# Performance work log

Hardware: AMD Instinct MI355X
Metric: run time of the kernel (lower is better)

Reference implementation:

```python
import jax, jax.numpy as jnp
import numpy as np

INPUT_DIM = 1024
HIDDEN_DIM = 2048
NUM_EMB = 4096
EMB_DIM = 256
N = 65536


def setup_inputs() -> dict:
    key = jax.random.key(0)
    ks = jax.random.split(key, 10)
    s = lambda fan_in: 1.0 / np.sqrt(fan_in)
    return {
        "x": jax.random.normal(ks[0], (N, INPUT_DIM), dtype=jnp.float32),
        # encoder: Linear(input_dim, hidden) -> ReLU -> Linear(hidden, emb)
        "W1": jax.random.uniform(ks[1], (INPUT_DIM, HIDDEN_DIM), jnp.float32, -s(INPUT_DIM), s(INPUT_DIM)),
        "b1": jax.random.uniform(ks[2], (HIDDEN_DIM,), jnp.float32, -s(INPUT_DIM), s(INPUT_DIM)),
        "W2": jax.random.uniform(ks[3], (HIDDEN_DIM, EMB_DIM), jnp.float32, -s(HIDDEN_DIM), s(HIDDEN_DIM)),
        "b2": jax.random.uniform(ks[4], (EMB_DIM,), jnp.float32, -s(HIDDEN_DIM), s(HIDDEN_DIM)),
        # codebook (nn.Embedding weight)
        "codebook": jax.random.normal(ks[5], (NUM_EMB, EMB_DIM), dtype=jnp.float32),
        # decoder: Linear(emb, hidden) -> ReLU -> Linear(hidden, input_dim)
        "W3": jax.random.uniform(ks[6], (EMB_DIM, HIDDEN_DIM), jnp.float32, -s(EMB_DIM), s(EMB_DIM)),
        "b3": jax.random.uniform(ks[7], (HIDDEN_DIM,), jnp.float32, -s(EMB_DIM), s(EMB_DIM)),
        "W4": jax.random.uniform(ks[8], (HIDDEN_DIM, INPUT_DIM), jnp.float32, -s(HIDDEN_DIM), s(HIDDEN_DIM)),
        "b4": jax.random.uniform(ks[9], (INPUT_DIM,), jnp.float32, -s(HIDDEN_DIM), s(HIDDEN_DIM)),
    }


def reference(x, W1, b1, W2, b2, codebook, W3, b3, W4, b4):
    # encoder
    h = jax.nn.relu(x @ W1 + b1)
    encoded = h @ W2 + b2                      # [N, E]
    # cdist (squared form; argmin is identical to Euclidean argmin)
    enc_sq = jnp.sum(encoded * encoded, axis=-1, keepdims=True)   # [N, 1]
    cb_sq = jnp.sum(codebook * codebook, axis=-1)                 # [K]
    d2 = enc_sq - 2.0 * (encoded @ codebook.T) + cb_sq            # [N, K]
    indices = jnp.argmin(d2, axis=-1)                             # [N]
    quantized = codebook[indices]                                 # [N, E]
    # decoder
    h2 = jax.nn.relu(quantized @ W3 + b3)
    decoded = h2 @ W4 + b4
    return (quantized, decoded)
```

## Files before the change

### kernel.cpp

```cpp
#include <hip/hip_runtime.h>

#define N_ROWS 65536
#define IN_DIM 1024
#define HID    2048
#define EMB    256
#define NCODE  4096

typedef __attribute__((ext_vector_type(8))) short bf16x8;
typedef __attribute__((ext_vector_type(4))) float f32x4;

__device__ __forceinline__ unsigned short f2bf(float v) {
    unsigned u = __float_as_uint(v);
    u += 0x7FFFu + ((u >> 16) & 1u);
    return (unsigned short)(u >> 16);
}
__device__ __forceinline__ float bf2f(unsigned short h) {
    return __uint_as_float(((unsigned)h) << 16);
}
__device__ __forceinline__ void gload16(const unsigned short* g, unsigned short* l) {
    __builtin_amdgcn_global_load_lds(
        (const __attribute__((address_space(1))) unsigned int*)g,
        (__attribute__((address_space(3))) unsigned int*)l, 16, 0, 0);
}

template<int SPLIT>
__global__ __launch_bounds__(256) void k_conv_w(
    const float* __restrict__ src, unsigned short* __restrict__ dh,
    unsigned short* __restrict__ dl, int NC, int nkt)
{
    const int t = threadIdx.x;
    const int nt = blockIdx.x, kt = blockIdx.y;
    const int kk = t >> 2, j4 = (t & 3) << 2;
    const int k0 = kt << 6, n0 = nt << 4;
    float4 v = *(const float4*)(src + (size_t)(k0 + kk) * NC + n0 + j4);
    size_t tb = ((size_t)nt * nkt + kt) * 1024 + ((kk >> 3) * 128) + (kk & 7);
    float vv[4] = {v.x, v.y, v.z, v.w};
    #pragma unroll
    for (int j = 0; j < 4; ++j) {
        unsigned short h = f2bf(vv[j]);
        dh[tb + (size_t)(j4 + j) * 8] = h;
        if (SPLIT) dl[tb + (size_t)(j4 + j) * 8] = f2bf(vv[j] - bf2f(h));
    }
}

__global__ __launch_bounds__(256) void k_conv_cb(
    const float* __restrict__ cb, unsigned short* __restrict__ ch,
    unsigned short* __restrict__ cl_, float* __restrict__ halfsq)
{
    const int t = threadIdx.x;
    const int ct = blockIdx.x;
    const int cl = t >> 4, f = t & 15;
    const int code = (ct << 4) + cl;
    float ssq = 0.f;
    #pragma unroll
    for (int it = 0; it < 4; ++it) {
        const int k4 = (f << 2) + (it << 6);
        float4 v = *(const float4*)(cb + (size_t)code * EMB + k4);
        ssq += v.x * v.x + v.y * v.y + v.z * v.z + v.w * v.w;
        size_t tb = ((size_t)(ct * 4 + (k4 >> 6))) * 1024 + ((k4 >> 3) & 7) * 128 + cl * 8 + (k4 & 7);
        ushort4 h = { f2bf(v.x), f2bf(v.y), f2bf(v.z), f2bf(v.w) };
        *(ushort4*)&ch[tb] = h;
        ushort4 lo = { f2bf(v.x - bf2f(h.x)), f2bf(v.y - bf2f(h.y)),
                       f2bf(v.z - bf2f(h.z)), f2bf(v.w - bf2f(h.w)) };
        *(ushort4*)&cl_[tb] = lo;
    }
    #pragma unroll
    for (int off = 1; off <= 8; off <<= 1) ssq += __shfl_xor(ssq, off);
    if (f == 0) halfsq[code] = 0.5f * ssq;
}

template<int SPLIT, int AFMT, int OUTT>
__global__ __launch_bounds__(512, 2) void k_layer2(
    const float* __restrict__ A, const unsigned short* __restrict__ At, int a_nkt,
    int lda, int K,
    const unsigned short* __restrict__ Bh, const unsigned short* __restrict__ Bl,
    int b_nkt, const float* __restrict__ bias, int biasoff,
    float* __restrict__ out, unsigned short* __restrict__ outt,
    int outw, int relu, int init, int ny_log2)
{
    constexpr int AL = 8192;
    constexpr int BH = SPLIT ? 16384 : 8192;
    __shared__ __align__(16) unsigned short s_mem[32768];

    const int t = threadIdx.x;
    const int id = blockIdx.x;
    const int m_low = id & 7, rest = id >> 3;
    const int nb = rest & ((1 << ny_log2) - 1);
    const int m0 = (((rest >> ny_log2) << 3) | m_low) * 128;
    const int nb0 = nb * 256;
    const int lane = t & 63, wv = t >> 6;
    const int wm = wv >> 2, wn = wv & 3;
    const int g = lane >> 4, rr = lane & 15;

    f32x4 acc[4][4];
    #pragma unroll
    for (int mi = 0; mi < 4; ++mi)
        #pragma unroll
        for (int ni = 0; ni < 4; ++ni) acc[mi][ni] = (f32x4){0.f, 0.f, 0.f, 0.f};

    for (int kc = 0; kc < K; kc += 64) {
        const int ktile = kc >> 6;
        #pragma unroll
        for (int jj = 0; jj < 2; ++jj) {
            const int j = wv * 2 + jj;
            const size_t gt = ((size_t)(nb0 / 16 + j) * b_nkt + ktile) * 1024;
            #pragma unroll
            for (int half = 0; half < 2; ++half)
                gload16(Bh + gt + half * 512 + lane * 8,
                        &s_mem[BH + j * 1024 + half * 512]);
        }
        if (AFMT == 0) {
            #pragma unroll
            for (int it = 0; it < 4; ++it) {
                int f = t + (it << 9);
                int r = f >> 4, k4 = (f & 15) << 2;
                float4 v = *(const float4*)(A + (size_t)(m0 + r) * lda + kc + k4);
                int mt = r >> 4, rl = r & 15, kb = k4 >> 3, e = k4 & 7;
                int addr = mt * 1024 + kb * 128 + ((rl ^ kb) << 3) + e;
                ushort4 hi, lo;
                hi.x = f2bf(v.x); hi.y = f2bf(v.y); hi.z = f2bf(v.z); hi.w = f2bf(v.w);
                *(ushort4*)&s_mem[addr] = hi;
                if (SPLIT) {
                    lo.x = f2bf(v.x - bf2f(hi.x)); lo.y = f2bf(v.y - bf2f(hi.y));
                    lo.z = f2bf(v.z - bf2f(hi.z)); lo.w = f2bf(v.w - bf2f(hi.w));
                    *(ushort4*)&s_mem[AL + addr] = lo;
                }
            }
        } else {
            const size_t gt = ((size_t)(m0 / 16 + wv) * a_nkt + ktile) * 1024;
            #pragma unroll
            for (int half = 0; half < 2; ++half)
                gload16(At + gt + half * 512 + lane * 8,
                        &s_mem[wv * 1024 + half * 512]);
        }
        __syncthreads();
        __builtin_amdgcn_s_setprio(1);
        #pragma unroll
        for (int s = 0; s < 2; ++s) {
            const int kb = (s << 2) + g;
            bf16x8 a_h[4], a_l[4], b_h[4], b_l[4];
            #pragma unroll
            for (int i = 0; i < 4; ++i) {
                int arow = (AFMT == 0) ? (((rr ^ kb) & 15) << 3) : (rr << 3);
                int aaddr = (wm * 4 + i) * 1024 + kb * 128 + arow;
                a_h[i] = *(const bf16x8*)&s_mem[aaddr];
                if (SPLIT) a_l[i] = *(const bf16x8*)&s_mem[AL + aaddr];
                int baddr = (wn * 4 + i) * 1024 + kb * 128 + (rr << 3);
                b_h[i] = *(const bf16x8*)&s_mem[BH + baddr];
                if (SPLIT)
                    b_l[i] = *(const bf16x8*)(Bl +
                        ((size_t)(nb0 / 16 + wn * 4 + i) * b_nkt + ktile) * 1024
                        + kb * 128 + (rr << 3));
            }
            #pragma unroll
            for (int mi = 0; mi < 4; ++mi)
                #pragma unroll
                for (int ni = 0; ni < 4; ++ni) {
                    acc[mi][ni] = __builtin_amdgcn_mfma_f32_16x16x32_bf16(a_h[mi], b_h[ni], acc[mi][ni], 0, 0, 0);
                    if (SPLIT) {
                        acc[mi][ni] = __builtin_amdgcn_mfma_f32_16x16x32_bf16(a_l[mi], b_h[ni], acc[mi][ni], 0, 0, 0);
                        acc[mi][ni] = __builtin_amdgcn_mfma_f32_16x16x32_bf16(a_h[mi], b_l[ni], acc[mi][ni], 0, 0, 0);
                    }
                }
        }
        __builtin_amdgcn_s_setprio(0);
        __syncthreads();
    }

    if (OUTT == 0) {
        float* sf = (float*)s_mem;
        for (int rm = 0; rm < 2; ++rm) {
            if (wm == rm) {
                #pragma unroll
                for (int mi = 0; mi < 4; ++mi)
                    #pragma unroll
                    for (int ni = 0; ni < 4; ++ni)
                        #pragma unroll
                        for (int rg = 0; rg < 4; ++rg)
                            sf[(mi * 16 + g * 4 + rg) * 256 + wn * 64 + ni * 16 + rr] = acc[mi][ni][rg];
            }
            __syncthreads();
            #pragma unroll
            for (int it = 0; it < 8; ++it) {
                int f = t + (it << 9);
                int r = f >> 6, c4 = (f & 63) << 2;
                float4 v = *(const float4*)&sf[r * 256 + c4];
                int gr = m0 + rm * 64 + r, gc = nb0 + c4;
                float* op = out + (size_t)gr * outw + gc;
                if (init) {
                    v.x += bias[biasoff + gc + 0]; v.y += bias[biasoff + gc + 1];
                    v.z += bias[biasoff + gc + 2]; v.w += bias[biasoff + gc + 3];
                } else {
                    float4 o = *(const float4*)op;
                    v.x += o.x; v.y += o.y; v.z += o.z; v.w += o.w;
                }
                if (relu) {
                    v.x = fmaxf(v.x, 0.f); v.y = fmaxf(v.y, 0.f);
                    v.z = fmaxf(v.z, 0.f); v.w = fmaxf(v.w, 0.f);
                }
                *(float4*)op = v;
            }
            __syncthreads();
        }
    } else {
        #pragma unroll
        for (int mi = 0; mi < 4; ++mi)
            #pragma unroll
            for (int ni = 0; ni < 4; ++ni) {
                const int c = wn * 64 + ni * 16 + rr;
                float bb = bias[biasoff + nb0 + c];
                #pragma unroll
                for (int rg = 0; rg < 4; ++rg) {
                    float v = acc[mi][ni][rg] + bb;
                    if (relu) v = fmaxf(v, 0.f);
                    int addr = ((wm * 4 + mi) * 4 + wn) * 1024
                             + (ni * 2 + (rr >> 3)) * 128 + (g * 4 + rg) * 8 + (rr & 7);
                    s_mem[addr] = f2bf(v);
                }
            }
        __syncthreads();
        #pragma unroll
        for (int it = 0; it < 8; ++it) {
            int f = t + (it << 9);
            int tl = f >> 7, w8 = f & 127;
            size_t gaddr = ((size_t)(m0 / 16 + (tl >> 2)) * outw + nb0 / 64 + (tl & 3)) * 1024;
            *(float4*)(outt + gaddr + w8 * 8) = *(const float4*)&s_mem[tl * 1024 + w8 * 8];
        }
    }
}

__global__ __launch_bounds__(512, 4) void k_dist(
    float* encq, const unsigned short* __restrict__ ch,
    const unsigned short* __restrict__ cl,
    const float* __restrict__ hsq, const float* __restrict__ cb)
{
    __shared__ __align__(16) unsigned short s_cb[2][16384];
    __shared__ int s_c1[128], s_c2[128];

    const int t = threadIdx.x;
    const int lane = t & 63, wv = t >> 6;
    const int g = lane >> 4, rr = lane & 15;
    const int r0 = blockIdx.x * 128;

    bf16x8 eh[8], el[8];
    {
        const float* ep = encq + (size_t)(r0 + wv * 16 + rr) * EMB + g * 8;
        #pragma unroll
        for (int s = 0; s < 8; ++s) {
            float4 v0 = *(const float4*)(ep + s * 32);
            float4 v1 = *(const float4*)(ep + s * 32 + 4);
            float vv[8] = {v0.x, v0.y, v0.z, v0.w, v1.x, v1.y, v1.z, v1.w};
            bf16x8 a, b;
            #pragma unroll
            for (int j = 0; j < 8; ++j) {
                unsigned short h = f2bf(vv[j]);
                a[j] = (short)h;
                b[j] = (short)f2bf(vv[j] - bf2f(h));
            }
            eh[s] = a; el[s] = b;
        }
    }
    float b1v[4], b2v[4]; int i1v[4], i2v[4];
    #pragma unroll
    for (int r2 = 0; r2 < 4; ++r2) { b1v[r2] = -1e30f; b2v[r2] = -1e30f; i1v[r2] = 0; i2v[r2] = 0; }

    #define STAGE(buf, c)                                                              \
        {                                                                              \
            const unsigned short* gh_ = ch + (size_t)(c) * 8192 + wv * 1024;           \
            const unsigned short* gl_ = cl + (size_t)(c) * 8192 + wv * 1024;           \
            _Pragma("unroll")                                                          \
            for (int i_ = 0; i_ < 2; ++i_) {                                           \
                gload16(gh_ + i_ * 512 + lane * 8, &s_cb[buf][wv * 1024 + i_ * 512]);  \
                gload16(gl_ + i_ * 512 + lane * 8, &s_cb[buf][8192 + wv * 1024 + i_ * 512]); \
            }                                                                          \
        }

    #define COMPUTE(cur, c, hv_)                                                       \
        {                                                                              \
            f32x4 ahh[2], ahl[2], alh[2];                                              \
            _Pragma("unroll")                                                          \
            for (int ci = 0; ci < 2; ++ci) {                                           \
                ahh[ci] = (f32x4){0.f, 0.f, 0.f, 0.f};                                 \
                ahl[ci] = (f32x4){0.f, 0.f, 0.f, 0.f};                                 \
                alh[ci] = (f32x4){0.f, 0.f, 0.f, 0.f};                                 \
            }                                                                          \
            __builtin_amdgcn_s_setprio(1);                                             \
            _Pragma("unroll")                                                          \
            for (int s = 0; s < 8; ++s) {                                              \
                const int ktile = s >> 1, kb = ((s & 1) << 2) + g;                     \
                _Pragma("unroll")                                                      \
                for (int ci = 0; ci < 2; ++ci) {                                       \
                    const int off = (ci * 4 + ktile) * 1024 + kb * 128 + rr * 8;       \
                    bf16x8 bh = *(const bf16x8*)&s_cb[cur][off];                       \
                    bf16x8 bl = *(const bf16x8*)&s_cb[cur][8192 + off];                \
                    ahh[ci] = __builtin_amdgcn_mfma_f32_16x16x32_bf16(eh[s], bh, ahh[ci], 0, 0, 0); \
                    ahl[ci] = __builtin_amdgcn_mfma_f32_16x16x32_bf16(eh[s], bl, ahl[ci], 0, 0, 0); \
                    alh[ci] = __builtin_amdgcn_mfma_f32_16x16x32_bf16(el[s], bh, alh[ci], 0, 0, 0); \
                }                                                                      \
            }                                                                          \
            __builtin_amdgcn_s_setprio(0);                                             \
            _Pragma("unroll")                                                          \
            for (int ci = 0; ci < 2; ++ci) {                                           \
                f32x4 av = ahh[ci] + ahl[ci] + alh[ci];                                \
                const int code = ((c) << 5) + (ci << 4) + rr;                          \
                const float hs = __shfl(hv_, ci * 16 + rr);                            \
                _Pragma("unroll")                                                      \
                for (int r2 = 0; r2 < 4; ++r2) {                                       \
                    float v = av[r2] - hs;                                             \
                    bool bt1 = (v > b1v[r2]) || (v == b1v[r2] && code < i1v[r2]);      \
                    bool bt2 = (v > b2v[r2]) || (v == b2v[r2] && code < i2v[r2]);      \
                    if (bt1) { b2v[r2] = b1v[r2]; i2v[r2] = i1v[r2]; b1v[r2] = v; i1v[r2] = code; } \
                    else if (bt2) { b2v[r2] = v; i2v[r2] = code; }                     \
                }                                                                      \
            }                                                                          \
        }

    STAGE(0, 0)
    int cur = 0;
    for (int c = 0; c < 127; ++c) {
        STAGE(cur ^ 1, c + 1)
        float hv_ = hsq[(c << 5) + (lane & 31)];
        asm volatile("s_waitcnt vmcnt(5)" ::: "memory");
        __builtin_amdgcn_s_barrier();
        __builtin_amdgcn_sched_barrier(0);
        COMPUTE(cur, c, hv_)
        asm volatile("" ::: "memory");
        __builtin_amdgcn_s_barrier();
        cur ^= 1;
    }
    {
        float hv_ = hsq[(127 << 5) + (lane & 31)];
        asm volatile("s_waitcnt vmcnt(0)" ::: "memory");
        __builtin_amdgcn_s_barrier();
        __builtin_amdgcn_sched_barrier(0);
        COMPUTE(cur, 127, hv_)
    }
    #undef STAGE
    #undef COMPUTE

    #pragma unroll
    for (int off = 1; off <= 8; off <<= 1) {
        #pragma unroll
        for (int r2 = 0; r2 < 4; ++r2) {
            float ob1 = __shfl_xor(b1v[r2], off), ob2 = __shfl_xor(b2v[r2], off);
            int oi1 = __shfl_xor(i1v[r2], off), oi2 = __shfl_xor(i2v[r2], off);
            bool ofirst = (ob1 > b1v[r2]) || (ob1 == b1v[r2] && oi1 < i1v[r2]);
            if (ofirst) {
                bool mysec = (b1v[r2] > ob2) || (b1v[r2] == ob2 && i1v[r2] < oi2);
                b2v[r2] = mysec ? b1v[r2] : ob2; i2v[r2] = mysec ? i1v[r2] : oi2;
                b1v[r2] = ob1; i1v[r2] = oi1;
            } else {
                bool osec = (ob1 > b2v[r2]) || (ob1 == b2v[r2] && oi1 < i2v[r2]);
                b2v[r2] = osec ? ob1 : b2v[r2]; i2v[r2] = osec ? oi1 : i2v[r2];
            }
        }
    }
    if (rr == 0) {
        #pragma unroll
        for (int r2 = 0; r2 < 4; ++r2) {
            int rl = wv * 16 + g * 4 + r2;
            s_c1[rl] = i1v[r2]; s_c2[rl] = i2v[r2];
        }
    }
    __syncthreads();

    for (int rloc = 0; rloc < 16; ++rloc) {
        const int row = wv * 16 + rloc;
        const int c1 = s_c1[row], c2 = s_c2[row];
        float4 ev = *(const float4*)(encq + (size_t)(r0 + row) * EMB + lane * 4);
        float4 v1 = *(const float4*)(cb + (size_t)c1 * EMB + lane * 4);
        float4 v2 = *(const float4*)(cb + (size_t)c2 * EMB + lane * 4);
        float d1 = ev.x * v1.x + ev.y * v1.y + ev.z * v1.z + ev.w * v1.w;
        float d2 = ev.x * v2.x + ev.y * v2.y + ev.z * v2.z + ev.w * v2.w;
        #pragma unroll
        for (int off = 1; off <= 32; off <<= 1) {
            d1 += __shfl_xor(d1, off);
            d2 += __shfl_xor(d2, off);
        }
        if (lane == 0) {
            float s1 = d1 - hsq[c1], s2 = d2 - hsq[c2];
            bool keep1 = (s1 > s2) || (s1 == s2 && c1 < c2);
            s_c1[row] = keep1 ? c1 : c2;
        }
    }
    __syncthreads();
    #pragma unroll
    for (int it = 0; it < 16; ++it) {
        int f = t + (it << 9);
        int row = f >> 6, c4 = (f & 63) << 2;
        int bi = s_c1[row];
        *(float4*)(encq + (size_t)(r0 + row) * EMB + c4) =
            *(const float4*)(cb + (size_t)bi * EMB + c4);
    }
}

__global__ __launch_bounds__(256) void k_dec_fb(
    const float* __restrict__ qz,
    const float* __restrict__ W3, const float* __restrict__ b3,
    const float* __restrict__ W4, const float* __restrict__ b4,
    float* __restrict__ outd) {
    __shared__ float s_q[8][EMB];
    __shared__ float s_h2[8][HID];
    const int t = threadIdx.x;
    const int row0 = blockIdx.x * 8;
    #pragma unroll
    for (int r = 0; r < 8; ++r) s_q[r][t] = qz[(size_t)(row0 + r) * EMB + t];
    __syncthreads();
    for (int gg = 0; gg < 8; ++gg) {
        const int j = (gg << 8) + t;
        float acc[8];
        #pragma unroll
        for (int r = 0; r < 8; ++r) acc[r] = 0.f;
        const float* wp = W3 + j;
        for (int e = 0; e < EMB; e += 4) {
            const float w0 = wp[(size_t)(e + 0) * HID];
            const float w1v = wp[(size_t)(e + 1) * HID];
            const float w2v = wp[(size_t)(e + 2) * HID];
            const float w3v = wp[(size_t)(e + 3) * HID];
            #pragma unroll
            for (int r = 0; r < 8; ++r) {
                const float4 qv = *reinterpret_cast<const float4*>(&s_q[r][e]);
                acc[r] = fmaf(qv.x, w0, acc[r]);
                acc[r] = fmaf(qv.y, w1v, acc[r]);
                acc[r] = fmaf(qv.z, w2v, acc[r]);
                acc[r] = fmaf(qv.w, w3v, acc[r]);
            }
        }
        const float bb = b3[j];
        #pragma unroll
        for (int r = 0; r < 8; ++r) s_h2[r][j] = fmaxf(acc[r] + bb, 0.f);
    }
    __syncthreads();
    float acc4[8][4];
    #pragma unroll
    for (int r = 0; r < 8; ++r)
        #pragma unroll
        for (int ci = 0; ci < 4; ++ci) acc4[r][ci] = 0.f;
    const float* w4p = W4 + t;
    for (int k = 0; k < HID; k += 4) {
        float wv[4][4];
        #pragma unroll
        for (int ki = 0; ki < 4; ++ki)
            #pragma unroll
            for (int ci = 0; ci < 4; ++ci)
                wv[ki][ci] = w4p[(size_t)(k + ki) * IN_DIM + (ci << 8)];
        #pragma unroll
        for (int r = 0; r < 8; ++r) {
            const float4 hv = *reinterpret_cast<const float4*>(&s_h2[r][k]);
            #pragma unroll
            for (int ci = 0; ci < 4; ++ci) {
                acc4[r][ci] = fmaf(hv.x, wv[0][ci], acc4[r][ci]);
                acc4[r][ci] = fmaf(hv.y, wv[1][ci], acc4[r][ci]);
                acc4[r][ci] = fmaf(hv.z, wv[2][ci], acc4[r][ci]);
                acc4[r][ci] = fmaf(hv.w, wv[3][ci], acc4[r][ci]);
            }
        }
    }
    #pragma unroll
    for (int ci = 0; ci < 4; ++ci) {
        const float bb = b4[(ci << 8) + t];
        #pragma unroll
        for (int r = 0; r < 8; ++r)
            outd[(size_t)(row0 + r) * IN_DIM + (ci << 8) + t] = acc4[r][ci] + bb;
    }
}

extern "C" void kernel_launch(void* const* d_in, const int* in_sizes, int n_in,
                              void* d_out, int out_size, void* d_ws, size_t ws_size,
                              hipStream_t stream) {
    const float* x  = (const float*)d_in[0];
    const float* W1 = (const float*)d_in[1];
    const float* b1 = (const float*)d_in[2];
    const float* W2 = (const float*)d_in[3];
    const float* b2 = (const float*)d_in[4];
    const float* cb = (const float*)d_in[5];
    const float* W3 = (const float*)d_in[6];
    const float* b3 = (const float*)d_in[7];
    const float* W4 = (const float*)d_in[8];
    const float* b4 = (const float*)d_in[9];

    float* outq = (float*)d_out;
    float* outd = outq + (size_t)N_ROWS * EMB;

    unsigned short* ou = (unsigned short*)outd;
    unsigned short* W1Th = ou;
    unsigned short* W1Tl = ou + 2097152;
    unsigned short* W2Th = ou + 4194304;
    unsigned short* W2Tl = ou + 4718592;
    unsigned short* cbh  = ou + 5242880;
    unsigned short* cbl  = ou + 6291456;
    float* halfsq = outd + 3670016;
    float* hbuf   = outd + 4194304;
    float* enc    = outq;

    const bool fastdec = ws_size >= (size_t)72351744;
    unsigned short* W3Th = (unsigned short*)d_ws;
    unsigned short* W4Th = W3Th + 524288;
    unsigned short* h2t  = (unsigned short*)((char*)d_ws + 5242880);

    k_conv_w<1><<<dim3(128, 16), 256, 0, stream>>>(W1, W1Th, W1Tl, HID, 16);
    k_conv_w<1><<<dim3(16, 32), 256, 0, stream>>>(W2, W2Th, W2Tl, EMB, 32);
    k_conv_cb<<<256, 256, 0, stream>>>(cb, cbh, cbl, halfsq);
    if (fastdec) {
        k_conv_w<0><<<dim3(128, 4), 256, 0, stream>>>(W3, W3Th, nullptr, HID, 4);
        k_conv_w<0><<<dim3(64, 32), 256, 0, stream>>>(W4, W4Th, nullptr, IN_DIM, 32);
    }
    for (int q = 0; q < 4; ++q) {
        k_layer2<1, 0, 0><<<1024, 512, 0, stream>>>(
            x, nullptr, 0, IN_DIM, IN_DIM,
            W1Th + (size_t)q * 524288, W1Tl + (size_t)q * 524288, 16,
            b1, q * 512, hbuf, nullptr, 512, 1, 1, 1);
        k_layer2<1, 0, 0><<<512, 512, 0, stream>>>(
            hbuf, nullptr, 0, 512, 512,
            W2Th + (size_t)q * 8192, W2Tl + (size_t)q * 8192, 32,
            b2, 0, enc, nullptr, EMB, 0, q == 0, 0);
    }
    k_dist<<<512, 512, 0, stream>>>(enc, cbh, cbl, halfsq, cb);
    if (fastdec) {
        for (int s = 0; s < 4; ++s) {
            const size_t roff = (size_t)s * 16384;
            k_layer2<0, 0, 1><<<1024, 512, 0, stream>>>(
                outq + roff * EMB, nullptr, 0, EMB, EMB,
                W3Th, nullptr, 4,
                b3, 0, nullptr, h2t, 32, 1, 0, 3);
            k_layer2<0, 1, 0><<<512, 512, 0, stream>>>(
                nullptr, h2t, 32, 0, HID,
                W4Th, nullptr, 32,
                b4, 0, outd + roff * IN_DIM, nullptr, IN_DIM, 0, 1, 2);
        }
    } else {
        k_dec_fb<<<N_ROWS / 8, 256, 0, stream>>>(outq, W3, b3, W4, b4, outd);
    }
}
```

Baseline: 2.487 ms.

## Process two row groups per wave in distance kernel to reuse codebook LDS reads

Each wave in k_dist now handles 32 rows (two 16-row groups) instead of 16, so every codebook fragment read from LDS feeds twice as many MFMAs. The block covers 256 rows and the grid is halved to 256 blocks. This cuts LDS traffic and codebook global loads per row. In exchange register use roughly doubles, occupancy drops to 2 blocks per CU, and with only 256 blocks there may be fewer waves than the GPU can keep busy.

```diff
diff --git a/kernel.cpp b/kernel.cpp
--- a/kernel.cpp
+++ b/kernel.cpp
@@ -229,22 +229,23 @@
     }
 }
 
-__global__ __launch_bounds__(512, 4) void k_dist(
+__global__ __launch_bounds__(512, 2) void k_dist(
     float* encq, const unsigned short* __restrict__ ch,
     const unsigned short* __restrict__ cl,
     const float* __restrict__ hsq, const float* __restrict__ cb)
 {
     __shared__ __align__(16) unsigned short s_cb[2][16384];
-    __shared__ int s_c1[128], s_c2[128];
+    __shared__ int s_c1[256], s_c2[256];
 
     const int t = threadIdx.x;
     const int lane = t & 63, wv = t >> 6;
     const int g = lane >> 4, rr = lane & 15;
-    const int r0 = blockIdx.x * 128;
-
-    bf16x8 eh[8], el[8];
-    {
-        const float* ep = encq + (size_t)(r0 + wv * 16 + rr) * EMB + g * 8;
+    const int r0 = blockIdx.x * 256;
+
+    bf16x8 eh[2][8], el[2][8];
+    #pragma unroll
+    for (int rg = 0; rg < 2; ++rg) {
+        const float* ep = encq + (size_t)(r0 + wv * 32 + rg * 16 + rr) * EMB + g * 8;
         #pragma unroll
         for (int s = 0; s < 8; ++s) {
             float4 v0 = *(const float4*)(ep + s * 32);
@@ -257,12 +258,17 @@
                 a[j] = (short)h;
                 b[j] = (short)f2bf(vv[j] - bf2f(h));
             }
-            eh[s] = a; el[s] = b;
-        }
-    }
-    float b1v[4], b2v[4]; int i1v[4], i2v[4];
-    #pragma unroll
-    for (int r2 = 0; r2 < 4; ++r2) { b1v[r2] = -1e30f; b2v[r2] = -1e30f; i1v[r2] = 0; i2v[r2] = 0; }
+            eh[rg][s] = a; el[rg][s] = b;
+        }
+    }
+    float b1v[2][4], b2v[2][4]; int i1v[2][4], i2v[2][4];
+    #pragma unroll
+    for (int rg = 0; rg < 2; ++rg)
+        #pragma unroll
+        for (int r2 = 0; r2 < 4; ++r2) {
+            b1v[rg][r2] = -1e30f; b2v[rg][r2] = -1e30f;
+            i1v[rg][r2] = 0; i2v[rg][r2] = 0;
+        }
 
     #define STAGE(buf, c)                                                              \
         {                                                                              \
@@ -277,13 +283,15 @@
 
     #define COMPUTE(cur, c, hv_)                                                       \
         {                                                                              \
-            f32x4 ahh[2], ahl[2], alh[2];                                              \
+            f32x4 ahh[2][2], ahl[2][2], alh[2][2];                                     \
             _Pragma("unroll")                                                          \
-            for (int ci = 0; ci < 2; ++ci) {                                           \
-                ahh[ci] = (f32x4){0.f, 0.f, 0.f, 0.f};                                 \
-                ahl[ci] = (f32x4){0.f, 0.f, 0.f, 0.f};                                 \
-                alh[ci] = (f32x4){0.f, 0.f, 0.f, 0.f};                                 \
-            }                                                                          \
+            for (int rg = 0; rg < 2; ++rg)                                             \
+                _Pragma("unroll")                                                      \
+                for (int ci = 0; ci < 2; ++ci) {                                       \
+                    ahh[rg][ci] = (f32x4){0.f, 0.f, 0.f, 0.f};                         \
+                    ahl[rg][ci] = (f32x4){0.f, 0.f, 0.f, 0.f};                         \
+                    alh[rg][ci] = (f32x4){0.f, 0.f, 0.f, 0.f};                         \
+                }                                                                      \
             __builtin_amdgcn_s_setprio(1);                                             \
             _Pragma("unroll")                                                          \
             for (int s = 0; s < 8; ++s) {                                              \
@@ -293,26 +301,32 @@
                     const int off = (ci * 4 + ktile) * 1024 + kb * 128 + rr * 8;       \
                     bf16x8 bh = *(const bf16x8*)&s_cb[cur][off];                       \
                     bf16x8 bl = *(const bf16x8*)&s_cb[cur][8192 + off];                \
-                    ahh[ci] = __builtin_amdgcn_mfma_f32_16x16x32_bf16(eh[s], bh, ahh[ci], 0, 0, 0); \
-                    ahl[ci] = __builtin_amdgcn_mfma_f32_16x16x32_bf16(eh[s], bl, ahl[ci], 0, 0, 0); \
-                    alh[ci] = __builtin_amdgcn_mfma_f32_16x16x32_bf16(el[s], bh, alh[ci], 0, 0, 0); \
+                    _Pragma("unroll")                                                  \
+                    for (int rg = 0; rg < 2; ++rg) {                                   \
+                        ahh[rg][ci] = __builtin_amdgcn_mfma_f32_16x16x32_bf16(eh[rg][s], bh, ahh[rg][ci], 0, 0, 0); \
+                        ahl[rg][ci] = __builtin_amdgcn_mfma_f32_16x16x32_bf16(eh[rg][s], bl, ahl[rg][ci], 0, 0, 0); \
+                        alh[rg][ci] = __builtin_amdgcn_mfma_f32_16x16x32_bf16(el[rg][s], bh, alh[rg][ci], 0, 0, 0); \
+                    }                                                                  \
                 }                                                                      \
             }                                                                          \
             __builtin_amdgcn_s_setprio(0);                                             \
             _Pragma("unroll")                                                          \
-            for (int ci = 0; ci < 2; ++ci) {                                           \
-                f32x4 av = ahh[ci] + ahl[ci] + alh[ci];                                \
-                const int code = ((c) << 5) + (ci << 4) + rr;                          \
-                const float hs = __shfl(hv_, ci * 16 + rr);                            \
+            for (int rg = 0; rg < 2; ++rg)                                             \
                 _Pragma("unroll")                                                      \
-                for (int r2 = 0; r2 < 4; ++r2) {                                       \
-                    float v = av[r2] - hs;                                             \
-                    bool bt1 = (v > b1v[r2]) || (v == b1v[r2] && code < i1v[r2]);      \
-                    bool bt2 = (v > b2v[r2]) || (v == b2v[r2] && code < i2v[r2]);      \
-                    if (bt1) { b2v[r2] = b1v[r2]; i2v[r2] = i1v[r2]; b1v[r2] = v; i1v[r2] = code; } \
-                    else if (bt2) { b2v[r2] = v; i2v[r2] = code; }                     \
+                for (int ci = 0; ci < 2; ++ci) {                                       \
+                    f32x4 av = ahh[rg][ci] + ahl[rg][ci] + alh[rg][ci];                \
+                    const int code = ((c) << 5) + (ci << 4) + rr;                      \
+                    const float hs = __shfl(hv_, ci * 16 + rr);                        \
+                    _Pragma("unroll")                                                  \
+                    for (int r2 = 0; r2 < 4; ++r2) {                                   \
+                        float v = av[r2] - hs;                                         \
+                        bool bt1 = (v > b1v[rg][r2]) || (v == b1v[rg][r2] && code < i1v[rg][r2]); \
+                        bool bt2 = (v > b2v[rg][r2]) || (v == b2v[rg][r2] && code < i2v[rg][r2]); \
+                        if (bt1) { b2v[rg][r2] = b1v[rg][r2]; i2v[rg][r2] = i1v[rg][r2]; \
+                                   b1v[rg][r2] = v; i1v[rg][r2] = code; }              \
+                        else if (bt2) { b2v[rg][r2] = v; i2v[rg][r2] = code; }         \
+                    }                                                                  \
                 }                                                                      \
-            }                                                                          \
         }
 
     STAGE(0, 0)
@@ -341,31 +355,35 @@
     #pragma unroll
     for (int off = 1; off <= 8; off <<= 1) {
         #pragma unroll
-        for (int r2 = 0; r2 < 4; ++r2) {
-            float ob1 = __shfl_xor(b1v[r2], off), ob2 = __shfl_xor(b2v[r2], off);
-            int oi1 = __shfl_xor(i1v[r2], off), oi2 = __shfl_xor(i2v[r2], off);
-            bool ofirst = (ob1 > b1v[r2]) || (ob1 == b1v[r2] && oi1 < i1v[r2]);
-            if (ofirst) {
-                bool mysec = (b1v[r2] > ob2) || (b1v[r2] == ob2 && i1v[r2] < oi2);
-                b2v[r2] = mysec ? b1v[r2] : ob2; i2v[r2] = mysec ? i1v[r2] : oi2;
-                b1v[r2] = ob1; i1v[r2] = oi1;
-            } else {
-                bool osec = (ob1 > b2v[r2]) || (ob1 == b2v[r2] && oi1 < i2v[r2]);
-                b2v[r2] = osec ? ob1 : b2v[r2]; i2v[r2] = osec ? oi1 : i2v[r2];
-            }
-        }
+        for (int rg = 0; rg < 2; ++rg)
+            #pragma unroll
+            for (int r2 = 0; r2 < 4; ++r2) {
+                float ob1 = __shfl_xor(b1v[rg][r2], off), ob2 = __shfl_xor(b2v[rg][r2], off);
+                int oi1 = __shfl_xor(i1v[rg][r2], off), oi2 = __shfl_xor(i2v[rg][r2], off);
+                bool ofirst = (ob1 > b1v[rg][r2]) || (ob1 == b1v[rg][r2] && oi1 < i1v[rg][r2]);
+                if (ofirst) {
+                    bool mysec = (b1v[rg][r2] > ob2) || (b1v[rg][r2] == ob2 && i1v[rg][r2] < oi2);
+                    b2v[rg][r2] = mysec ? b1v[rg][r2] : ob2; i2v[rg][r2] = mysec ? i1v[rg][r2] : oi2;
+                    b1v[rg][r2] = ob1; i1v[rg][r2] = oi1;
+                } else {
+                    bool osec = (ob1 > b2v[rg][r2]) || (ob1 == b2v[rg][r2] && oi1 < i2v[rg][r2]);
+                    b2v[rg][r2] = osec ? ob1 : b2v[rg][r2]; i2v[rg][r2] = osec ? oi1 : i2v[rg][r2];
+                }
+            }
     }
     if (rr == 0) {
         #pragma unroll
-        for (int r2 = 0; r2 < 4; ++r2) {
-            int rl = wv * 16 + g * 4 + r2;
-            s_c1[rl] = i1v[r2]; s_c2[rl] = i2v[r2];
-        }
+        for (int rg = 0; rg < 2; ++rg)
+            #pragma unroll
+            for (int r2 = 0; r2 < 4; ++r2) {
+                int rl = wv * 32 + rg * 16 + g * 4 + r2;
+                s_c1[rl] = i1v[rg][r2]; s_c2[rl] = i2v[rg][r2];
+            }
     }
     __syncthreads();
 
-    for (int rloc = 0; rloc < 16; ++rloc) {
-        const int row = wv * 16 + rloc;
+    for (int rloc = 0; rloc < 32; ++rloc) {
+        const int row = wv * 32 + rloc;
         const int c1 = s_c1[row], c2 = s_c2[row];
         float4 ev = *(const float4*)(encq + (size_t)(r0 + row) * EMB + lane * 4);
         float4 v1 = *(const float4*)(cb + (size_t)c1 * EMB + lane * 4);
@@ -385,7 +403,7 @@
     }
     __syncthreads();
     #pragma unroll
-    for (int it = 0; it < 16; ++it) {
+    for (int it = 0; it < 32; ++it) {
         int f = t + (it << 9);
         int row = f >> 6, c4 = (f & 63) << 2;
         int bi = s_c1[row];
@@ -515,7 +533,7 @@
             W2Th + (size_t)q * 8192, W2Tl + (size_t)q * 8192, 32,
             b2, 0, enc, nullptr, EMB, 0, q == 0, 0);
     }
-    k_dist<<<512, 512, 0, stream>>>(enc, cbh, cbl, halfsq, cb);
+    k_dist<<<256, 512, 0, stream>>>(enc, cbh, cbl, halfsq, cb);
     if (fastdec) {
         for (int s = 0; s < 4; ++s) {
             const size_t roff = (size_t)s * 16384;
```

New measurement: 2.452 ms. No clear change (-1.4%).
